# Kernel optimization log

Measured on AMD Instinct MI355X. Metric: run time of the kernel, lower is better.

The kernel has to match this reference:

```python
import jax, jax.numpy as jnp
import numpy as np

B, T, S, D = 8, 512, 512, 1024
NUM_HEADS = 16
REUSE_HEADS = 8
NEW_HEADS = NUM_HEADS - REUSE_HEADS
KEY_DIM = 64
VALUE_DIM = 64
PE_MAX = 512  # pe_max_seq_length


def setup_inputs() -> dict:
    key = jax.random.key(0)
    ks = jax.random.split(key, 12)
    s = 0.02
    return {
        "query": jax.random.normal(ks[0], (B, T, D), jnp.float32),
        "value": jax.random.normal(ks[1], (B, S, D), jnp.float32),
        # scores reused from a previous layer (already softmaxed there)
        "reuse_attention_scores": jax.random.uniform(ks[2], (B, REUSE_HEADS, T, S), jnp.float32),
        "Wq": jax.random.normal(ks[3], (D, NEW_HEADS, KEY_DIM), jnp.float32) * s,
        "bq": jnp.zeros((NEW_HEADS, KEY_DIM), jnp.float32),
        "Wk": jax.random.normal(ks[4], (D, NEW_HEADS, KEY_DIM), jnp.float32) * s,
        "bk": jnp.zeros((NEW_HEADS, KEY_DIM), jnp.float32),
        "Wv": jax.random.normal(ks[5], (D, NUM_HEADS, VALUE_DIM), jnp.float32) * s,
        "bv": jnp.zeros((NUM_HEADS, VALUE_DIM), jnp.float32),
        # relative position embeddings: [1, new_heads, 2*PE_MAX - 1]
        "pos_emb": jax.random.truncated_normal(ks[6], -2.0, 2.0, (1, NEW_HEADS, 2 * PE_MAX - 1), jnp.float32) * 0.2,
        # output denses: one for reused heads (no bias), one for new heads (bias)
        "Wo_reuse": jax.random.normal(ks[7], (REUSE_HEADS, VALUE_DIM, D), jnp.float32) * s,
        "Wo_new": jax.random.normal(ks[8], (NEW_HEADS, VALUE_DIM, D), jnp.float32) * s,
        "bo": jnp.zeros((D,), jnp.float32),
    }


def reference(query, value, reuse_attention_scores, Wq, bq, Wk, bk, Wv, bv,
              pos_emb, Wo_reuse, Wo_new, bo):
    # projections (EinsumDense abc,cde->abde + bias over last two dims)
    q = jnp.einsum("btd,dnh->btnh", query, Wq) + bq           # [B,T,Hn,kd]
    k = jnp.einsum("bsd,dnh->bsnh", value, Wk) + bk           # [B,S,Hn,kd]
    v = jnp.einsum("bsd,dnh->bsnh", value, Wv) + bv           # [B,S,H,vd]
    v_reuse, v_new = v[:, :, :REUSE_HEADS, :], v[:, :, REUSE_HEADS:, :]

    # new-head scores: scaled QK^T  (dot_product_equation 'aecd,abcd->acbe')
    q = q * (1.0 / np.sqrt(float(KEY_DIM)))
    new_scores = jnp.einsum("bsnh,btnh->bnts", k, q)          # [B,Hn,T,S]

    # relative position bias: index = clip(key_pos - query_pos + PE_MAX-1)
    rel = jnp.arange(S)[None, :] - jnp.arange(T)[:, None] + (PE_MAX - 1)
    rel = jnp.clip(rel, 0, 2 * PE_MAX - 2)                    # [T,S]
    bias = pos_emb[0][:, rel]                                 # [Hn,T,S]
    new_scores = jax.nn.softmax(new_scores + bias[None], axis=-1)

    # reused heads consume previous-layer scores directly (dropout=0)
    reuse_scores = reuse_attention_scores[:, :REUSE_HEADS]
    out_reuse = jnp.einsum("bnts,bsnh->btnh", reuse_scores, v_reuse)
    out_new = jnp.einsum("bnts,bsnh->btnh", new_scores, v_new)

    # separate output projections, summed; bias only on the new-heads dense
    out = (jnp.einsum("btnh,nhd->btd", out_reuse, Wo_reuse)
           + jnp.einsum("btnh,nhd->btd", out_new, Wo_new) + bo)
    return out
```

## Files before the change

kernel.cpp:

```cpp
#include <hip/hip_runtime.h>
#include <hip/hip_bf16.h>

typedef __bf16 bf16_t;
typedef __bf16 bf16x8 __attribute__((ext_vector_type(8)));
typedef float  f32x4  __attribute__((ext_vector_type(4)));

enum { EPI_NONE = 0, EPI_BIASN = 1, EPI_REL = 2 };

#define GLDS(gsrc, ldst)                                                              \
  __builtin_amdgcn_global_load_lds(                                                   \
      (const __attribute__((address_space(1))) unsigned int*)(gsrc),                  \
      (__attribute__((address_space(3))) unsigned int*)(ldst), 16, 0, 0)

__global__ void k_convert2(const float* __restrict__ a, bf16_t* __restrict__ da,
                           const float* __restrict__ b, bf16_t* __restrict__ db, int n8) {
  int i = blockIdx.x * blockDim.x + threadIdx.x;
  const float* s; bf16_t* d;
  if (i < n8) { s = a; d = da; } else { s = b; d = db; i -= n8; }
  const float4* p = reinterpret_cast<const float4*>(s) + 2 * (long)i;
  float4 x = p[0], y = p[1];
  bf16x8 o;
  o[0] = (bf16_t)x.x; o[1] = (bf16_t)x.y; o[2] = (bf16_t)x.z; o[3] = (bf16_t)x.w;
  o[4] = (bf16_t)y.x; o[5] = (bf16_t)y.y; o[6] = (bf16_t)y.z; o[7] = (bf16_t)y.w;
  reinterpret_cast<bf16x8*>(d)[i] = o;
}

struct TArgs {
  const float* src[5];
  bf16_t* dst[5];
  int C[5], Ct[5], off[5], blk0[6];
  float scale[5];
};
__global__ void k_transpose5(TArgs ta) {
  __shared__ float tile[32][33];
  const int bid = blockIdx.x;
  int s = 0;
  while (bid >= ta.blk0[s + 1]) ++s;
  const int bi = bid - ta.blk0[s];
  const int Ct = ta.Ct[s];
  const int c0 = (bi % Ct) * 32, r0 = (bi / Ct) * 32;
  const int C = ta.C[s];
  const float* src = ta.src[s];
  const int lx = threadIdx.x & 31, ly = threadIdx.x >> 5;
  #pragma unroll
  for (int i = 0; i < 32; i += 8)
    tile[ly + i][lx] = src[(long)(r0 + ly + i) * C + (c0 + lx)];
  __syncthreads();
  const float sc = ta.scale[s];
  bf16_t* dst = ta.dst[s];
  const int off = ta.off[s];
  #pragma unroll
  for (int i = 0; i < 32; i += 8)
    dst[(long)(c0 + ly + i) * 1024 + off + (r0 + lx)] = (bf16_t)(tile[lx][ly + i] * sc);
}

template<int MI, int EPI, bool OUT_F32>
__global__ __launch_bounds__(256)
void k_gemm_st(const bf16_t* __restrict__ A_, const bf16_t* __restrict__ B_,
               void* __restrict__ C_, const float* __restrict__ bias,
               int K, int lda, int ldb, int ldc,
               int ZN, long sAb, long sAn, long sBb, long sBn, long sCb, long sCn) {
  __shared__ bf16_t lsA[MI * 1024];
  __shared__ bf16_t lsB[4096];
  const int z = blockIdx.z, zb = z / ZN, zn = z - zb * ZN;
  const int t = threadIdx.x, lane = t & 63, wid = t >> 6;
  const int wr = wid >> 1, wc = wid & 1;
  const int m0 = blockIdx.x * (MI * 32), n0 = blockIdx.y * 128;
  const int lhi = lane >> 4, llo = lane & 15;

  const bf16_t* Ab = A_ + zb * sAb + zn * sAn + (long)m0 * lda;
  const bf16_t* Bb = B_ + zb * sBb + zn * sBn + (long)n0 * ldb;

  const int e0 = t * 8,        r0s = e0 >> 5, c0s = e0 & 31;
  const int e1 = (256 + t) * 8, r1s = e1 >> 5, c1s = e1 & 31;
  bf16_t* lA0 = lsA + wid * 512;
  bf16_t* lA1 = lsA + 2048 + wid * 512;
  bf16_t* lB0 = lsB + wid * 512;
  bf16_t* lB1 = lsB + 2048 + wid * 512;

  f32x4 acc[MI][4] = {};

  for (int k0 = 0; k0 < K; k0 += 32) {
    GLDS(Ab + (long)r0s * lda + k0 + c0s, lA0);
    if constexpr (MI == 4) GLDS(Ab + (long)r1s * lda + k0 + c1s, lA1);
    GLDS(Bb + (long)r0s * ldb + k0 + c0s, lB0);
    GLDS(Bb + (long)r1s * ldb + k0 + c1s, lB1);
    __syncthreads();
    bf16x8 a[MI], b[4];
    #pragma unroll
    for (int mi = 0; mi < MI; ++mi)
      a[mi] = *reinterpret_cast<const bf16x8*>(lsA + (wr * (MI * 16) + mi * 16 + llo) * 32 + lhi * 8);
    #pragma unroll
    for (int ni = 0; ni < 4; ++ni)
      b[ni] = *reinterpret_cast<const bf16x8*>(lsB + (wc * 64 + ni * 16 + llo) * 32 + lhi * 8);
    #pragma unroll
    for (int mi = 0; mi < MI; ++mi)
      #pragma unroll
      for (int ni = 0; ni < 4; ++ni)
        acc[mi][ni] = __builtin_amdgcn_mfma_f32_16x16x32_bf16(a[mi], b[ni], acc[mi][ni], 0, 0, 0);
    __syncthreads();
  }

  float* Cf = (float*)C_;
  bf16_t* Cb = (bf16_t*)C_;
  const long coff = zb * sCb + zn * sCn;
  #pragma unroll
  for (int mi = 0; mi < MI; ++mi) {
    #pragma unroll
    for (int ni = 0; ni < 4; ++ni) {
      #pragma unroll
      for (int r = 0; r < 4; ++r) {
        const int m = m0 + wr * (MI * 16) + mi * 16 + lhi * 4 + r;
        const int n = n0 + wc * 64 + ni * 16 + llo;
        float v = acc[mi][ni][r];
        if constexpr (EPI == EPI_BIASN) v += bias[n];
        if constexpr (OUT_F32) Cf[coff + (long)m * ldc + n] = v;
        else                   Cb[coff + (long)m * ldc + n] = (bf16_t)v;
      }
    }
  }
}

struct ProjItem {
  const bf16_t* A; const bf16_t* B; bf16_t* C; const float* bias;
  float bscale; int ldc; int Nt; int writeT;
};
struct ProjArgs { ProjItem it[3]; };

__global__ __launch_bounds__(256)
void k_gemm_proj(ProjArgs pa) {
  const ProjItem it = pa.it[blockIdx.z];
  if ((int)blockIdx.y >= it.Nt) return;
  __shared__ bf16_t lsA[4096];
  __shared__ bf16_t lsB[4096];
  const int t = threadIdx.x, lane = t & 63, wid = t >> 6;
  const int wr = wid >> 1, wc = wid & 1;
  const int m0 = blockIdx.x * 128, n0 = blockIdx.y * 128;
  const int lhi = lane >> 4, llo = lane & 15;

  const bf16_t* Ab = it.A + (long)m0 * 1024;
  const bf16_t* Bb = it.B + (long)n0 * 1024;

  const int e0 = t * 8,        r0s = e0 >> 5, c0s = e0 & 31;
  const int e1 = (256 + t) * 8, r1s = e1 >> 5, c1s = e1 & 31;
  bf16_t* lA0 = lsA + wid * 512;
  bf16_t* lA1 = lsA + 2048 + wid * 512;
  bf16_t* lB0 = lsB + wid * 512;
  bf16_t* lB1 = lsB + 2048 + wid * 512;

  f32x4 acc[4][4] = {};

  for (int k0 = 0; k0 < 1024; k0 += 32) {
    GLDS(Ab + (long)r0s * 1024 + k0 + c0s, lA0);
    GLDS(Ab + (long)r1s * 1024 + k0 + c1s, lA1);
    GLDS(Bb + (long)r0s * 1024 + k0 + c0s, lB0);
    GLDS(Bb + (long)r1s * 1024 + k0 + c1s, lB1);
    __syncthreads();
    bf16x8 a[4], b[4];
    #pragma unroll
    for (int mi = 0; mi < 4; ++mi)
      a[mi] = *reinterpret_cast<const bf16x8*>(lsA + (wr * 64 + mi * 16 + llo) * 32 + lhi * 8);
    #pragma unroll
    for (int ni = 0; ni < 4; ++ni)
      b[ni] = *reinterpret_cast<const bf16x8*>(lsB + (wc * 64 + ni * 16 + llo) * 32 + lhi * 8);
    #pragma unroll
    for (int mi = 0; mi < 4; ++mi)
      #pragma unroll
      for (int ni = 0; ni < 4; ++ni)
        acc[mi][ni] = __builtin_amdgcn_mfma_f32_16x16x32_bf16(a[mi], b[ni], acc[mi][ni], 0, 0, 0);
    __syncthreads();
  }

  #pragma unroll
  for (int mi = 0; mi < 4; ++mi) {
    #pragma unroll
    for (int ni = 0; ni < 4; ++ni) {
      #pragma unroll
      for (int r = 0; r < 4; ++r) {
        const int m = m0 + wr * 64 + mi * 16 + lhi * 4 + r;
        const int n = n0 + wc * 64 + ni * 16 + llo;
        float v = acc[mi][ni][r] + it.bias[n] * it.bscale;
        if (it.writeT) it.C[(long)n * it.ldc + m] = (bf16_t)v;
        else           it.C[(long)m * it.ldc + n] = (bf16_t)v;
      }
    }
  }
}

__global__ __launch_bounds__(256, 2)
void k_fattn(const bf16_t* __restrict__ qb, const bf16_t* __restrict__ kb,
             const bf16_t* __restrict__ vbT, const float* __restrict__ pe,
             bf16_t* __restrict__ om) {
  __shared__ float pes[1024];
  __shared__ bf16_t Kt[128 * 64];
  __shared__ bf16_t Vt[64 * 128];
  __shared__ bf16_t Pt[4][16 * 128];

  const int bid = blockIdx.x;
  const int tt = bid >> 6;
  const int bh = bid & 63;
  const int b = bh >> 3, h = bh & 7;
  const int lane = threadIdx.x & 63, w = threadIdx.x >> 6;
  const int lhi = lane >> 4, llo = lane & 15;
  const int t0w = tt * 64 + w * 16;

  char* KtB = (char*)Kt;
  char* VtB = (char*)Vt;
  char* PtB = (char*)Pt + w * 4096;

  const bf16_t* Ksrc = kb + (long)(b * 512) * 512 + h * 64;
  const bf16_t* Vsrc = vbT + (long)(512 + h * 64) * 4096 + b * 512;
  const int krow = w * 32 + (lane >> 3);
  const int kcol = ((lane & 7) ^ (lane >> 3)) << 3;
  const int vn   = w * 16 + (lane >> 4);
  bf16_t* kdst = (bf16_t*)(KtB + w * 4096);
  bf16_t* vdst = (bf16_t*)(VtB + w * 4096);

#define STAGE_K(it_)                                                                   \
  { _Pragma("unroll")                                                                  \
    for (int g = 0; g < 4; ++g)                                                        \
      GLDS(Ksrc + (long)((it_) * 128 + krow + g * 8) * 512 + kcol, kdst + g * 512); }
#define STAGE_V(it_)                                                                   \
  { _Pragma("unroll")                                                                  \
    for (int g = 0; g < 4; ++g)                                                        \
      GLDS(Vsrc + (long)(vn + g * 4) * 4096 + (it_) * 128 +                            \
               (((lane & 15) ^ (g * 4 + (lane >> 4))) << 3),                           \
           vdst + g * 512); }

  STAGE_K(0);
  STAGE_V(0);

  const bf16_t* Qb = qb + (long)(b * 512 + t0w + llo) * 512 + h * 64;
  bf16x8 qf0 = *reinterpret_cast<const bf16x8*>(Qb + lhi * 8);
  bf16x8 qf1 = *reinterpret_cast<const bf16x8*>(Qb + 32 + lhi * 8);
  for (int i = threadIdx.x; i < 1023; i += 256) pes[i] = pe[h * 1023 + i];

  f32x4 oacc[4] = {};
  float lr[4] = {0.f, 0.f, 0.f, 0.f};

  __syncthreads();

  for (int it = 0; it < 4; ++it) {
    const int s0 = it * 128;

    f32x4 acc[8] = {};
    #pragma unroll
    for (int st = 0; st < 8; ++st) {
      const int rowb = st * 16 + llo;
      const int sw = (rowb & 7) << 4;
      bf16x8 kf0 = *reinterpret_cast<const bf16x8*>(KtB + rowb * 128 + ((lhi * 16) ^ sw));
      bf16x8 kf1 = *reinterpret_cast<const bf16x8*>(KtB + rowb * 128 + ((64 + lhi * 16) ^ sw));
      acc[st] = __builtin_amdgcn_mfma_f32_16x16x32_bf16(qf0, kf0, acc[st], 0, 0, 0);
      acc[st] = __builtin_amdgcn_mfma_f32_16x16x32_bf16(qf1, kf1, acc[st], 0, 0, 0);
    }

    __syncthreads();
    if (it < 3) STAGE_K(it + 1);

    #pragma unroll
    for (int r = 0; r < 4; ++r) {
      const int tl = lhi * 4 + r;
      const int bidx = s0 + llo - (t0w + tl) + 511;
      const int swp = (tl & 15) << 4;
      float lp = 0.f;
      #pragma unroll
      for (int st = 0; st < 8; ++st) {
        const float e = __expf(acc[st][r] + pes[bidx + st * 16]);
        lp += e;
        *reinterpret_cast<bf16_t*>(PtB + tl * 256 + (((st * 16 + llo) * 2) ^ swp)) = (bf16_t)e;
      }
      lr[r] += lp;
    }

    const int swa = llo << 4;
    #pragma unroll
    for (int ks = 0; ks < 4; ++ks) {
      bf16x8 pa = *reinterpret_cast<const bf16x8*>(PtB + llo * 256 + ((ks * 64 + lhi * 16) ^ swa));
      #pragma unroll
      for (int ni = 0; ni < 4; ++ni) {
        const int rowv = ni * 16 + llo;
        bf16x8 vf = *reinterpret_cast<const bf16x8*>(VtB + rowv * 256 + ((ks * 64 + lhi * 16) ^ swa));
        oacc[ni] = __builtin_amdgcn_mfma_f32_16x16x32_bf16(pa, vf, oacc[ni], 0, 0, 0);
      }
    }

    __syncthreads();
    if (it < 3) STAGE_V(it + 1);
  }

  #pragma unroll
  for (int r = 0; r < 4; ++r) {
    lr[r] += __shfl_xor(lr[r], 1);
    lr[r] += __shfl_xor(lr[r], 2);
    lr[r] += __shfl_xor(lr[r], 4);
    lr[r] += __shfl_xor(lr[r], 8);
  }

  bf16_t* Ob = om + (long)(b * 512 + t0w + lhi * 4) * 1024 + 512 + h * 64;
  #pragma unroll
  for (int ni = 0; ni < 4; ++ni)
    #pragma unroll
    for (int r = 0; r < 4; ++r)
      Ob[(long)r * 1024 + ni * 16 + llo] = (bf16_t)(oacc[ni][r] * (1.f / lr[r]));
#undef STAGE_K
#undef STAGE_V
}

__global__ __launch_bounds__(256, 3)
void k_pvr(const float* __restrict__ reuse, const bf16_t* __restrict__ vbT,
           bf16_t* __restrict__ om) {
  __shared__ float red[2][32][68];
  const int z = blockIdx.y;
  const int b = z >> 3, head = z & 7;
  const int lane = threadIdx.x & 63, w = threadIdx.x >> 6;
  const int lhi = lane >> 4, llo = lane & 15;
  const int m0 = blockIdx.x * 32;
  const int ks0 = w * 128;

  const float*  Af = reuse + (long)b * 2097152 + (long)head * 262144;
  const bf16_t* Bp = vbT + (long)(head * 64) * 4096 + b * 512;

  f32x4 acc[2][4] = {};
  float4 Ax[2][2][2];
  bf16x8 Bx[2][4];

  #define PV_LOAD(kq, buf)                                                              \
    {                                                                                   \
      const int kk = ks0 + (kq) * 32 + lhi * 8;                                         \
      _Pragma("unroll")                                                                 \
      for (int mi = 0; mi < 2; ++mi) {                                                  \
        const float4* p = reinterpret_cast<const float4*>(Af + (long)(m0 + mi * 16 + llo) * 512 + kk); \
        Ax[buf][mi][0] = p[0];                                                          \
        Ax[buf][mi][1] = p[1];                                                          \
      }                                                                                 \
      _Pragma("unroll")                                                                 \
      for (int ni = 0; ni < 4; ++ni)                                                    \
        Bx[buf][ni] = *reinterpret_cast<const bf16x8*>(Bp + (long)(ni * 16 + llo) * 4096 + kk); \
    }

  PV_LOAD(0, 0);
  #pragma unroll
  for (int kq = 0; kq < 4; ++kq) {
    const int cb = kq & 1;
    if (kq < 3) {
      const int nb = (kq + 1) & 1;
      PV_LOAD(kq + 1, nb);
    }
    bf16x8 a[2];
    #pragma unroll
    for (int mi = 0; mi < 2; ++mi) {
      float4 x = Ax[cb][mi][0], y = Ax[cb][mi][1];
      bf16x8 tv;
      tv[0] = (bf16_t)x.x; tv[1] = (bf16_t)x.y; tv[2] = (bf16_t)x.z; tv[3] = (bf16_t)x.w;
      tv[4] = (bf16_t)y.x; tv[5] = (bf16_t)y.y; tv[6] = (bf16_t)y.z; tv[7] = (bf16_t)y.w;
      a[mi] = tv;
    }
    #pragma unroll
    for (int mi = 0; mi < 2; ++mi)
      #pragma unroll
      for (int ni = 0; ni < 4; ++ni)
        acc[mi][ni] = __builtin_amdgcn_mfma_f32_16x16x32_bf16(a[mi], Bx[cb][ni], acc[mi][ni], 0, 0, 0);
  }
  #undef PV_LOAD

  if (w >= 2) {
    #pragma unroll
    for (int mi = 0; mi < 2; ++mi)
      #pragma unroll
      for (int ni = 0; ni < 4; ++ni)
        #pragma unroll
        for (int r = 0; r < 4; ++r)
          red[w - 2][mi * 16 + lhi * 4 + r][ni * 16 + llo] = acc[mi][ni][r];
  }
  __syncthreads();
  if (w < 2) {
    #pragma unroll
    for (int mi = 0; mi < 2; ++mi)
      #pragma unroll
      for (int ni = 0; ni < 4; ++ni)
        #pragma unroll
        for (int r = 0; r < 4; ++r)
          acc[mi][ni][r] += red[w][mi * 16 + lhi * 4 + r][ni * 16 + llo];
  }
  __syncthreads();
  if (w == 1) {
    #pragma unroll
    for (int mi = 0; mi < 2; ++mi)
      #pragma unroll
      for (int ni = 0; ni < 4; ++ni)
        #pragma unroll
        for (int r = 0; r < 4; ++r)
          red[0][mi * 16 + lhi * 4 + r][ni * 16 + llo] = acc[mi][ni][r];
  }
  __syncthreads();
  if (w == 0) {
    bf16_t* Cb = om + (long)b * 524288 + head * 64;
    #pragma unroll
    for (int mi = 0; mi < 2; ++mi) {
      #pragma unroll
      for (int ni = 0; ni < 4; ++ni) {
        #pragma unroll
        for (int r = 0; r < 4; ++r) {
          const int m = m0 + mi * 16 + lhi * 4 + r;
          const int nn = ni * 16 + llo;
          float v = acc[mi][ni][r] + red[0][mi * 16 + lhi * 4 + r][nn];
          Cb[(long)m * 1024 + nn] = (bf16_t)v;
        }
      }
    }
  }
}

extern "C" void kernel_launch(void* const* d_in, const int* in_sizes, int n_in,
                              void* d_out, int out_size, void* d_ws, size_t ws_size,
                              hipStream_t stream) {
  const float* query = (const float*)d_in[0];
  const float* value = (const float*)d_in[1];
  const float* reuse = (const float*)d_in[2];
  const float* Wq    = (const float*)d_in[3];
  const float* bq    = (const float*)d_in[4];
  const float* Wk    = (const float*)d_in[5];
  const float* bk    = (const float*)d_in[6];
  const float* Wv    = (const float*)d_in[7];
  const float* bv    = (const float*)d_in[8];
  const float* pe    = (const float*)d_in[9];
  const float* WoR   = (const float*)d_in[10];
  const float* WoN   = (const float*)d_in[11];
  const float* bo    = (const float*)d_in[12];
  float* out = (float*)d_out;
  (void)in_sizes; (void)n_in; (void)out_size; (void)ws_size;

  char* w = (char*)d_ws;
  bf16_t* qx  = (bf16_t*)(w);
  bf16_t* vx  = (bf16_t*)(w + (8L  << 20));
  bf16_t* WqT = (bf16_t*)(w + (16L << 20));
  bf16_t* WkT = (bf16_t*)(w + (17L << 20));
  bf16_t* WvT = (bf16_t*)(w + (18L << 20));
  bf16_t* WoT = (bf16_t*)(w + (20L << 20));
  bf16_t* qb  = (bf16_t*)(w + (22L << 20));
  bf16_t* kb  = (bf16_t*)(w + (26L << 20));
  bf16_t* vbT = (bf16_t*)(w + (30L << 20));
  bf16_t* om  = (bf16_t*)(w + (38L << 20));

  k_convert2<<<4096, 256, 0, stream>>>(query, qx, value, vx, 524288);

  TArgs ta;
  ta.src[0] = Wq;  ta.dst[0] = WqT; ta.C[0] = 512;  ta.Ct[0] = 16; ta.off[0] = 0;   ta.scale[0] = 0.125f;
  ta.src[1] = Wk;  ta.dst[1] = WkT; ta.C[1] = 512;  ta.Ct[1] = 16; ta.off[1] = 0;   ta.scale[1] = 1.f;
  ta.src[2] = Wv;  ta.dst[2] = WvT; ta.C[2] = 1024; ta.Ct[2] = 32; ta.off[2] = 0;   ta.scale[2] = 1.f;
  ta.src[3] = WoR; ta.dst[3] = WoT; ta.C[3] = 1024; ta.Ct[3] = 32; ta.off[3] = 0;   ta.scale[3] = 1.f;
  ta.src[4] = WoN; ta.dst[4] = WoT; ta.C[4] = 1024; ta.Ct[4] = 32; ta.off[4] = 512; ta.scale[4] = 1.f;
  ta.blk0[0] = 0; ta.blk0[1] = 512; ta.blk0[2] = 1024; ta.blk0[3] = 2048; ta.blk0[4] = 2560; ta.blk0[5] = 3072;
  k_transpose5<<<3072, 256, 0, stream>>>(ta);

  ProjArgs pa;
  pa.it[0] = { qx, WqT, qb,  bq, 0.125f, 512,  4, 0 };
  pa.it[1] = { vx, WkT, kb,  bk, 1.f,    512,  4, 0 };
  pa.it[2] = { vx, WvT, vbT, bv, 1.f,    4096, 8, 1 };
  k_gemm_proj<<<dim3(32, 8, 3), 256, 0, stream>>>(pa);

  k_fattn<<<dim3(512), 256, 0, stream>>>(qb, kb, vbT, pe, om);

  k_pvr<<<dim3(16, 64), 256, 0, stream>>>(reuse, vbT, om);

  k_gemm_st<2, EPI_BIASN, true><<<dim3(64, 8, 1), 256, 0, stream>>>(
      om, WoT, out, bo, 1024, 1024, 1024, 1024, 1,
      0L, 0L, 0L, 0L, 0L, 0L);
}
```

Baseline: 109.9 us.

## Stage GEMM and attention epilogues through LDS for coalesced vector stores

Epilogues of the projection GEMM, the fused attention, the reuse PV kernel and the output GEMM now write accumulators into padded LDS tiles, then issue 16-byte coalesced global stores. Before, each lane wrote scattered scalar bf16/f32 elements, and the transposed V write was strided. The projection launch is flattened to a 1D grid of exactly 512 blocks, so the empty blocks that used to early-exit are gone. The change adds extra LDS traffic and barriers in each epilogue.

```diff
diff --git a/kernel.cpp b/kernel.cpp
--- a/kernel.cpp
+++ b/kernel.cpp
@@ -4,8 +4,6 @@
 typedef __bf16 bf16_t;
 typedef __bf16 bf16x8 __attribute__((ext_vector_type(8)));
 typedef float  f32x4  __attribute__((ext_vector_type(4)));
-
-enum { EPI_NONE = 0, EPI_BIASN = 1, EPI_REL = 2 };
 
 #define GLDS(gsrc, ldst)                                                              \
   __builtin_amdgcn_global_load_lds(                                                   \
@@ -54,22 +52,29 @@
     dst[(long)(c0 + ly + i) * 1024 + off + (r0 + lx)] = (bf16_t)(tile[lx][ly + i] * sc);
 }
 
-template<int MI, int EPI, bool OUT_F32>
+struct ProjItem {
+  const bf16_t* A; const bf16_t* B; bf16_t* C; const float* bias;
+  float bscale; int ldc; int writeT;
+};
+struct ProjArgs { ProjItem it[3]; };
+
 __global__ __launch_bounds__(256)
-void k_gemm_st(const bf16_t* __restrict__ A_, const bf16_t* __restrict__ B_,
-               void* __restrict__ C_, const float* __restrict__ bias,
-               int K, int lda, int ldb, int ldc,
-               int ZN, long sAb, long sAn, long sBb, long sBn, long sCb, long sCn) {
-  __shared__ bf16_t lsA[MI * 1024];
-  __shared__ bf16_t lsB[4096];
-  const int z = blockIdx.z, zb = z / ZN, zn = z - zb * ZN;
+void k_gemm_proj(ProjArgs pa) {
+  __shared__ char smem[18432];
+  bf16_t* lsA = (bf16_t*)smem;
+  bf16_t* lsB = (bf16_t*)(smem + 8192);
+
+  const int bid = blockIdx.x;
+  const int z = bid < 128 ? 0 : (bid < 256 ? 1 : 2);
+  const int local = bid - (z == 0 ? 0 : (z == 1 ? 128 : 256));
+  const ProjItem it = pa.it[z];
   const int t = threadIdx.x, lane = t & 63, wid = t >> 6;
   const int wr = wid >> 1, wc = wid & 1;
-  const int m0 = blockIdx.x * (MI * 32), n0 = blockIdx.y * 128;
+  const int m0 = (local & 31) * 128, n0 = (local >> 5) * 128;
   const int lhi = lane >> 4, llo = lane & 15;
 
-  const bf16_t* Ab = A_ + zb * sAb + zn * sAn + (long)m0 * lda;
-  const bf16_t* Bb = B_ + zb * sBb + zn * sBn + (long)n0 * ldb;
+  const bf16_t* Ab = it.A + (long)m0 * 1024;
+  const bf16_t* Bb = it.B + (long)n0 * 1024;
 
   const int e0 = t * 8,        r0s = e0 >> 5, c0s = e0 & 31;
   const int e1 = (256 + t) * 8, r1s = e1 >> 5, c1s = e1 & 31;
@@ -78,76 +83,6 @@
   bf16_t* lB0 = lsB + wid * 512;
   bf16_t* lB1 = lsB + 2048 + wid * 512;
 
-  f32x4 acc[MI][4] = {};
-
-  for (int k0 = 0; k0 < K; k0 += 32) {
-    GLDS(Ab + (long)r0s * lda + k0 + c0s, lA0);
-    if constexpr (MI == 4) GLDS(Ab + (long)r1s * lda + k0 + c1s, lA1);
-    GLDS(Bb + (long)r0s * ldb + k0 + c0s, lB0);
-    GLDS(Bb + (long)r1s * ldb + k0 + c1s, lB1);
-    __syncthreads();
-    bf16x8 a[MI], b[4];
-    #pragma unroll
-    for (int mi = 0; mi < MI; ++mi)
-      a[mi] = *reinterpret_cast<const bf16x8*>(lsA + (wr * (MI * 16) + mi * 16 + llo) * 32 + lhi * 8);
-    #pragma unroll
-    for (int ni = 0; ni < 4; ++ni)
-      b[ni] = *reinterpret_cast<const bf16x8*>(lsB + (wc * 64 + ni * 16 + llo) * 32 + lhi * 8);
-    #pragma unroll
-    for (int mi = 0; mi < MI; ++mi)
-      #pragma unroll
-      for (int ni = 0; ni < 4; ++ni)
-        acc[mi][ni] = __builtin_amdgcn_mfma_f32_16x16x32_bf16(a[mi], b[ni], acc[mi][ni], 0, 0, 0);
-    __syncthreads();
-  }
-
-  float* Cf = (float*)C_;
-  bf16_t* Cb = (bf16_t*)C_;
-  const long coff = zb * sCb + zn * sCn;
-  #pragma unroll
-  for (int mi = 0; mi < MI; ++mi) {
-    #pragma unroll
-    for (int ni = 0; ni < 4; ++ni) {
-      #pragma unroll
-      for (int r = 0; r < 4; ++r) {
-        const int m = m0 + wr * (MI * 16) + mi * 16 + lhi * 4 + r;
-        const int n = n0 + wc * 64 + ni * 16 + llo;
-        float v = acc[mi][ni][r];
-        if constexpr (EPI == EPI_BIASN) v += bias[n];
-        if constexpr (OUT_F32) Cf[coff + (long)m * ldc + n] = v;
-        else                   Cb[coff + (long)m * ldc + n] = (bf16_t)v;
-      }
-    }
-  }
-}
-
-struct ProjItem {
-  const bf16_t* A; const bf16_t* B; bf16_t* C; const float* bias;
-  float bscale; int ldc; int Nt; int writeT;
-};
-struct ProjArgs { ProjItem it[3]; };
-
-__global__ __launch_bounds__(256)
-void k_gemm_proj(ProjArgs pa) {
-  const ProjItem it = pa.it[blockIdx.z];
-  if ((int)blockIdx.y >= it.Nt) return;
-  __shared__ bf16_t lsA[4096];
-  __shared__ bf16_t lsB[4096];
-  const int t = threadIdx.x, lane = t & 63, wid = t >> 6;
-  const int wr = wid >> 1, wc = wid & 1;
-  const int m0 = blockIdx.x * 128, n0 = blockIdx.y * 128;
-  const int lhi = lane >> 4, llo = lane & 15;
-
-  const bf16_t* Ab = it.A + (long)m0 * 1024;
-  const bf16_t* Bb = it.B + (long)n0 * 1024;
-
-  const int e0 = t * 8,        r0s = e0 >> 5, c0s = e0 & 31;
-  const int e1 = (256 + t) * 8, r1s = e1 >> 5, c1s = e1 & 31;
-  bf16_t* lA0 = lsA + wid * 512;
-  bf16_t* lA1 = lsA + 2048 + wid * 512;
-  bf16_t* lB0 = lsB + wid * 512;
-  bf16_t* lB1 = lsB + 2048 + wid * 512;
-
   f32x4 acc[4][4] = {};
 
   for (int k0 = 0; k0 < 1024; k0 += 32) {
@@ -172,18 +107,136 @@
   }
 
   #pragma unroll
-  for (int mi = 0; mi < 4; ++mi) {
+  for (int mi = 0; mi < 4; ++mi)
     #pragma unroll
     for (int ni = 0; ni < 4; ++ni) {
-      #pragma unroll
-      for (int r = 0; r < 4; ++r) {
-        const int m = m0 + wr * 64 + mi * 16 + lhi * 4 + r;
-        const int n = n0 + wc * 64 + ni * 16 + llo;
-        float v = acc[mi][ni][r] + it.bias[n] * it.bscale;
-        if (it.writeT) it.C[(long)n * it.ldc + m] = (bf16_t)v;
-        else           it.C[(long)m * it.ldc + n] = (bf16_t)v;
+      const float bv = it.bias[n0 + wc * 64 + ni * 16 + llo] * it.bscale;
+      #pragma unroll
+      for (int r = 0; r < 4; ++r) acc[mi][ni][r] += bv;
+    }
+
+  if (!it.writeT) {
+    bf16_t* E = (bf16_t*)smem;
+    #pragma unroll
+    for (int p = 0; p < 2; ++p) {
+      if (wr == p) {
+        #pragma unroll
+        for (int mi = 0; mi < 4; ++mi)
+          #pragma unroll
+          for (int ni = 0; ni < 4; ++ni)
+            #pragma unroll
+            for (int r = 0; r < 4; ++r)
+              E[(mi * 16 + lhi * 4 + r) * 136 + wc * 64 + ni * 16 + llo] = (bf16_t)acc[mi][ni][r];
       }
-    }
+      __syncthreads();
+      #pragma unroll
+      for (int round = 0; round < 4; ++round) {
+        const int row = (t >> 4) + round * 16;
+        const int l16 = t & 15;
+        float4 v = *reinterpret_cast<const float4*>((char*)E + row * 272 + l16 * 16);
+        *reinterpret_cast<float4*>(it.C + (long)(m0 + p * 64 + row) * it.ldc + n0 + l16 * 8) = v;
+      }
+      __syncthreads();
+    }
+  } else {
+    bf16_t* E = (bf16_t*)smem;
+    #pragma unroll
+    for (int p = 0; p < 2; ++p) {
+      if (wr == p) {
+        #pragma unroll
+        for (int mi = 0; mi < 4; ++mi)
+          #pragma unroll
+          for (int ni = 0; ni < 4; ++ni)
+            #pragma unroll
+            for (int r = 0; r < 4; ++r)
+              E[(wc * 64 + ni * 16 + llo) * 72 + mi * 16 + lhi * 4 + r] = (bf16_t)acc[mi][ni][r];
+      }
+      __syncthreads();
+      #pragma unroll
+      for (int round = 0; round < 4; ++round) {
+        const int nr = (t >> 3) + round * 32;
+        const int l8 = t & 7;
+        float4 v = *reinterpret_cast<const float4*>((char*)E + nr * 144 + l8 * 16);
+        *reinterpret_cast<float4*>(it.C + (long)(n0 + nr) * it.ldc + m0 + p * 64 + l8 * 8) = v;
+      }
+      __syncthreads();
+    }
+  }
+}
+
+__global__ __launch_bounds__(256)
+void k_gemm_out(const bf16_t* __restrict__ A_, const bf16_t* __restrict__ B_,
+                float* __restrict__ C_, const float* __restrict__ bias) {
+  __shared__ char smem[16896];
+  bf16_t* lsA = (bf16_t*)smem;
+  bf16_t* lsB = (bf16_t*)(smem + 4096);
+
+  const int t = threadIdx.x, lane = t & 63, wid = t >> 6;
+  const int wr = wid >> 1, wc = wid & 1;
+  const int m0 = blockIdx.x * 64, n0 = blockIdx.y * 128;
+  const int lhi = lane >> 4, llo = lane & 15;
+
+  const bf16_t* Ab = A_ + (long)m0 * 1024;
+  const bf16_t* Bb = B_ + (long)n0 * 1024;
+
+  const int e0 = t * 8,        r0s = e0 >> 5, c0s = e0 & 31;
+  const int e1 = (256 + t) * 8, r1s = e1 >> 5, c1s = e1 & 31;
+  bf16_t* lA0 = lsA + wid * 512;
+  bf16_t* lB0 = lsB + wid * 512;
+  bf16_t* lB1 = lsB + 2048 + wid * 512;
+
+  f32x4 acc[2][4] = {};
+
+  for (int k0 = 0; k0 < 1024; k0 += 32) {
+    GLDS(Ab + (long)r0s * 1024 + k0 + c0s, lA0);
+    GLDS(Bb + (long)r0s * 1024 + k0 + c0s, lB0);
+    GLDS(Bb + (long)r1s * 1024 + k0 + c1s, lB1);
+    __syncthreads();
+    bf16x8 a[2], b[4];
+    #pragma unroll
+    for (int mi = 0; mi < 2; ++mi)
+      a[mi] = *reinterpret_cast<const bf16x8*>(lsA + (wr * 32 + mi * 16 + llo) * 32 + lhi * 8);
+    #pragma unroll
+    for (int ni = 0; ni < 4; ++ni)
+      b[ni] = *reinterpret_cast<const bf16x8*>(lsB + (wc * 64 + ni * 16 + llo) * 32 + lhi * 8);
+    #pragma unroll
+    for (int mi = 0; mi < 2; ++mi)
+      #pragma unroll
+      for (int ni = 0; ni < 4; ++ni)
+        acc[mi][ni] = __builtin_amdgcn_mfma_f32_16x16x32_bf16(a[mi], b[ni], acc[mi][ni], 0, 0, 0);
+    __syncthreads();
+  }
+
+  #pragma unroll
+  for (int mi = 0; mi < 2; ++mi)
+    #pragma unroll
+    for (int ni = 0; ni < 4; ++ni) {
+      const float bv = bias[n0 + wc * 64 + ni * 16 + llo];
+      #pragma unroll
+      for (int r = 0; r < 4; ++r) acc[mi][ni][r] += bv;
+    }
+
+  float* E = (float*)smem;
+  #pragma unroll
+  for (int p = 0; p < 2; ++p) {
+    if (wr == p) {
+      #pragma unroll
+      for (int mi = 0; mi < 2; ++mi)
+        #pragma unroll
+        for (int ni = 0; ni < 4; ++ni)
+          #pragma unroll
+          for (int r = 0; r < 4; ++r)
+            E[(mi * 16 + lhi * 4 + r) * 132 + wc * 64 + ni * 16 + llo] = acc[mi][ni][r];
+    }
+    __syncthreads();
+    #pragma unroll
+    for (int round = 0; round < 4; ++round) {
+      const int row = (t >> 5) + round * 8;
+      const int l32 = t & 31;
+      float4 v = *reinterpret_cast<const float4*>((char*)E + row * 528 + l32 * 16);
+      *reinterpret_cast<float4*>(C_ + (long)(m0 + p * 32 + row) * 1024 + n0 + l32 * 4) = v;
+    }
+    __syncthreads();
   }
 }
 
@@ -296,12 +349,19 @@
     lr[r] += __shfl_xor(lr[r], 8);
   }
 
-  bf16_t* Ob = om + (long)(b * 512 + t0w + lhi * 4) * 1024 + 512 + h * 64;
+  bf16_t* Ew = (bf16_t*)PtB;
   #pragma unroll
   for (int ni = 0; ni < 4; ++ni)
     #pragma unroll
     for (int r = 0; r < 4; ++r)
-      Ob[(long)r * 1024 + ni * 16 + llo] = (bf16_t)(oacc[ni][r] * (1.f / lr[r]));
+      Ew[(lhi * 4 + r) * 72 + ni * 16 + llo] = (bf16_t)(oacc[ni][r] * (1.f / lr[r]));
+  #pragma unroll
+  for (int round = 0; round < 2; ++round) {
+    const int lr8 = (lane >> 3) + round * 8;
+    const int l8 = lane & 7;
+    float4 v = *reinterpret_cast<const float4*>((char*)Ew + lr8 * 144 + l8 * 16);
+    *reinterpret_cast<float4*>(om + (long)(b * 512 + t0w + lr8) * 1024 + 512 + h * 64 + l8 * 8) = v;
+  }
 #undef STAGE_K
 #undef STAGE_V
 }
@@ -394,19 +454,24 @@
   }
   __syncthreads();
   if (w == 0) {
+    bf16_t* E = (bf16_t*)&red[1][0][0];
+    #pragma unroll
+    for (int mi = 0; mi < 2; ++mi)
+      #pragma unroll
+      for (int ni = 0; ni < 4; ++ni)
+        #pragma unroll
+        for (int r = 0; r < 4; ++r) {
+          const int mr = mi * 16 + lhi * 4 + r;
+          const int nn = ni * 16 + llo;
+          E[mr * 72 + nn] = (bf16_t)(acc[mi][ni][r] + red[0][mr][nn]);
+        }
     bf16_t* Cb = om + (long)b * 524288 + head * 64;
     #pragma unroll
-    for (int mi = 0; mi < 2; ++mi) {
-      #pragma unroll
-      for (int ni = 0; ni < 4; ++ni) {
-        #pragma unroll
-        for (int r = 0; r < 4; ++r) {
-          const int m = m0 + mi * 16 + lhi * 4 + r;
-          const int nn = ni * 16 + llo;
-          float v = acc[mi][ni][r] + red[0][mi * 16 + lhi * 4 + r][nn];
-          Cb[(long)m * 1024 + nn] = (bf16_t)v;
-        }
-      }
+    for (int round = 0; round < 4; ++round) {
+      const int row = (lane >> 3) + round * 8;
+      const int l8 = lane & 7;
+      float4 v = *reinterpret_cast<const float4*>((char*)E + row * 144 + l8 * 16);
+      *reinterpret_cast<float4*>(Cb + (long)(m0 + row) * 1024 + l8 * 8) = v;
     }
   }
 }
@@ -454,16 +519,14 @@
   k_transpose5<<<3072, 256, 0, stream>>>(ta);
 
   ProjArgs pa;
-  pa.it[0] = { qx, WqT, qb,  bq, 0.125f, 512,  4, 0 };
-  pa.it[1] = { vx, WkT, kb,  bk, 1.f,    512,  4, 0 };
-  pa.it[2] = { vx, WvT, vbT, bv, 1.f,    4096, 8, 1 };
-  k_gemm_proj<<<dim3(32, 8, 3), 256, 0, stream>>>(pa);
+  pa.it[0] = { qx, WqT, qb,  bq, 0.125f, 512,  0 };
+  pa.it[1] = { vx, WkT, kb,  bk, 1.f,    512,  0 };
+  pa.it[2] = { vx, WvT, vbT, bv, 1.f,    4096, 1 };
+  k_gemm_proj<<<dim3(512), 256, 0, stream>>>(pa);
 
   k_fattn<<<dim3(512), 256, 0, stream>>>(qb, kb, vbT, pe, om);
 
   k_pvr<<<dim3(16, 64), 256, 0, stream>>>(reuse, vbT, om);
 
-  k_gemm_st<2, EPI_BIASN, true><<<dim3(64, 8, 1), 256, 0, stream>>>(
-      om, WoT, out, bo, 1024, 1024, 1024, 1024, 1,
-      0L, 0L, 0L, 0L, 0L, 0L);
-}
+  k_gemm_out<<<dim3(64, 8), 256, 0, stream>>>(om, WoT, out, bo);
+}
```

Measured after the change: 99.35 us. -9.6%, faster.
